# Kernel tuning notes

Measured on AMD Instinct MI355X. Metric: run time of the kernel, lower is better.

## Reference

```python
import jax, jax.numpy as jnp
import numpy as np

N_HEAD = 16
SPARSITY_K = 64


def _apply_rope(x):
    # x: [B, H, T, D]
    D = x.shape[-1]
    T = x.shape[-2]
    freqs = 1.0 / (10000.0 ** (jnp.arange(0, D, 2, dtype=jnp.float32) / D))  # [D/2]
    angles = jnp.arange(T, dtype=jnp.float32)[:, None] * freqs[None, :]      # [T, D/2]
    cos, sin = jnp.cos(angles), jnp.sin(angles)
    xe, xo = x[..., ::2], x[..., 1::2]
    re = xe * cos - xo * sin
    ro = xe * sin + xo * cos
    return jnp.stack([re, ro], axis=-1).reshape(x.shape)


def _sparse_mask(route_weights, T, k):
    # Per head h, per query t: keep positions j<=t whose route score is among
    # the top-k of route_weights[h, 0:t+1] (tie-break by smaller index, like topk).
    s = route_weights[:, :T]                      # [H, T]
    idx = jnp.arange(T)
    # G[h, jp, j] = 1 if position jp beats position j in the top-k ordering
    G = (s[:, :, None] > s[:, None, :]) | ((s[:, :, None] == s[:, None, :]) & (idx[:, None] < idx[None, :]))
    rank = jnp.cumsum(G.astype(jnp.int32), axis=1)  # rank[h, t, j] = #{jp<=t beating j}
    causal = idx[None, :, None] >= idx[None, None, :]  # j <= t
    return causal & (rank < k)                    # [H, T, T] bool


def reference(x, W_attn, b_attn, W_proj, b_proj, route_weights):
    B, T, C = x.shape
    H = N_HEAD
    D = C // H
    qkv = x @ W_attn + b_attn                     # [B, T, 3C]
    q, k, v = jnp.split(qkv, 3, axis=-1)

    def heads(t):
        return t.reshape(B, T, H, D).transpose(0, 2, 1, 3)  # [B, H, T, D]

    q, k, v = heads(q), heads(k), heads(v)
    q = _apply_rope(q)
    k = _apply_rope(k)

    scores = jnp.einsum('bhtd,bhsd->bhts', q, k) / jnp.sqrt(jnp.float32(D))
    mask = _sparse_mask(route_weights, T, SPARSITY_K)       # [H, T, T]
    scores = jnp.where(mask[None], scores, -jnp.inf)
    attn = jax.nn.softmax(scores, axis=-1)                  # dropout off (eval mode)
    out = jnp.einsum('bhts,bhsd->bhtd', attn, v)
    out = out.transpose(0, 2, 1, 3).reshape(B, T, C)
    return out @ W_proj + b_proj


def setup_inputs() -> dict:
    key = jax.random.key(0)
    ks = jax.random.split(key, 6)
    B, T, C, H = 2, 2048, 2048, 16
    return {
        'x': jax.random.normal(ks[0], (B, T, C), dtype=jnp.float32),
        'W_attn': jax.random.normal(ks[1], (C, 3 * C), dtype=jnp.float32) * 0.02,
        'b_attn': jnp.zeros((3 * C,), dtype=jnp.float32),
        'W_proj': jax.random.normal(ks[2], (C, C), dtype=jnp.float32) * 0.02,
        'b_proj': jnp.zeros((C,), dtype=jnp.float32),
        'route_weights': jax.random.normal(ks[3], (H, T), dtype=jnp.float32) * 0.02,
    }
```

## Files before the change

### kernel.cpp

```cpp
#include <hip/hip_runtime.h>
#include <stdint.h>

#define B_ 2
#define T_ 2048
#define C_ 2048
#define H_ 16
#define D_ 128
#define KSP 64
#define C3 6144

typedef __attribute__((ext_vector_type(4))) float f32x4;
typedef __attribute__((ext_vector_type(8))) _Float16 f16x8;
typedef __attribute__((ext_vector_type(4))) _Float16 f16x4;
typedef __attribute__((ext_vector_type(2))) _Float16 f16x2;

__device__ __forceinline__ void gload16(const void* g, void* l) {
  __builtin_amdgcn_global_load_lds(
      (__attribute__((address_space(1))) void*)(uintptr_t)g,
      (__attribute__((address_space(3))) void*)(uint32_t)(uintptr_t)l,
      16, 0, 0);
}

__global__ __launch_bounds__(256) void k_prep(const float* __restrict__ x,
                                              _Float16* __restrict__ x16,
                                              const float* __restrict__ Wa,
                                              _Float16* __restrict__ WaT,
                                              const float* __restrict__ Wp,
                                              _Float16* __restrict__ WpT) {
  __shared__ float tile[32][33];
  const int b = blockIdx.x;
  const int tid = threadIdx.x;
  if (b < 2048) {
    const int base = b * 4096;
#pragma unroll
    for (int p = 0; p < 4; ++p) {
      const int i = base + p * 1024 + tid * 4;
      const float4 v = *(const float4*)(x + i);
      f16x4 o;
      o.x = (_Float16)v.x; o.y = (_Float16)v.y; o.z = (_Float16)v.z; o.w = (_Float16)v.w;
      *(f16x4*)(x16 + i) = o;
    }
    return;
  }
  const float* W;
  _Float16* WT;
  int n0, k0, N;
  if (b < 14336) {
    const int t = b - 2048;
    W = Wa; WT = WaT; N = C3;
    n0 = (t % 192) * 32;
    k0 = (t / 192) * 32;
  } else {
    const int t = b - 14336;
    W = Wp; WT = WpT; N = C_;
    n0 = (t % 64) * 32;
    k0 = (t / 64) * 32;
  }
  const int tx = tid & 31, ty = tid >> 5;
#pragma unroll
  for (int r = 0; r < 4; ++r)
    tile[ty + r * 8][tx] = W[(size_t)(k0 + ty + r * 8) * N + n0 + tx];
  __syncthreads();
#pragma unroll
  for (int r = 0; r < 4; ++r)
    WT[(size_t)(n0 + ty + r * 8) * C_ + k0 + tx] = (_Float16)tile[tx][ty + r * 8];
}

template <int F16OUT, int NJ, int ROPE>
__global__ __launch_bounds__(512) void k_gemm256(const _Float16* __restrict__ A,
                                                 const _Float16* __restrict__ BT,
                                                 const float* __restrict__ bias,
                                                 void* __restrict__ Cout,
                                                 int M, int N, int K,
                                                 int RGC, int RH, int CW) {
  constexpr int BN = 64 * NJ;
  __shared__ __align__(16) _Float16 sA[2][256 * 64];
  __shared__ __align__(16) _Float16 sB[2][BN * 64];
  const int tid = threadIdx.x;
  const int lane = tid & 63;
  const int wid = tid >> 6;
  const int wr = wid >> 2;
  const int wc = wid & 3;
  const int lr = lane & 15;
  const int g = lane >> 4;
  const int rot = lr & 7;
  const int bid = blockIdx.x;
  const int x = bid & 7, q = bid >> 3;
  const int bm = (x / RGC) * RH + q / CW;
  const int bn = (x % RGC) * CW + q % CW;
  const size_t arow0 = (size_t)bm * 256;
  const size_t brow0 = (size_t)bn * BN;

  f32x4 acc[8][NJ];
#pragma unroll
  for (int mi = 0; mi < 8; ++mi)
#pragma unroll
    for (int nj = 0; nj < NJ; ++nj) acc[mi][nj] = (f32x4){0.f, 0.f, 0.f, 0.f};

  auto STAGE_A = [&](int slot, int k0) {
    const int rord[4] = {0, 2, 1, 3};
#pragma unroll
    for (int ri = 0; ri < 4; ++ri) {
      const int u = tid + rord[ri] * 512;
      const int row = u >> 3, grl = u & 7;
      const int grn = (grl - (row & 7)) & 7;
      gload16(A + (arow0 + row) * K + k0 + grn * 8, &sA[slot][u * 8]);
    }
  };
  auto STAGE_B = [&](int slot, int k0) {
#pragma unroll
    for (int r = 0; r < NJ; ++r) {
      const int u = tid + r * 512;
      const int row = u >> 3, grl = u & 7;
      const int grn = (grl - (row & 7)) & 7;
      gload16(BT + (brow0 + row) * K + k0 + grn * 8, &sB[slot][u * 8]);
    }
  };

  f16x8 af[4], bf[NJ];
  auto LDA = [&](int slot, int mh, int kk) {
#pragma unroll
    for (int mi = 0; mi < 4; ++mi) {
      const int row = wr * 128 + (mh * 4 + mi) * 16 + lr;
      af[mi] = *(const f16x8*)&sA[slot][row * 64 + (((kk * 4 + g + rot) & 7) << 3)];
    }
  };
  auto LDB = [&](int slot, int kk) {
#pragma unroll
    for (int nj = 0; nj < NJ; ++nj) {
      const int row = wc * (16 * NJ) + nj * 16 + lr;
      bf[nj] = *(const f16x8*)&sB[slot][row * 64 + (((kk * 4 + g + rot) & 7) << 3)];
    }
  };
  auto MFMAB = [&](int mh) {
    __builtin_amdgcn_s_setprio(1);
#pragma unroll
    for (int mi = 0; mi < 4; ++mi)
#pragma unroll
      for (int nj = 0; nj < NJ; ++nj)
        acc[mh * 4 + mi][nj] =
            __builtin_amdgcn_mfma_f32_16x16x32_f16(af[mi], bf[nj], acc[mh * 4 + mi][nj], 0, 0, 0);
    __builtin_amdgcn_s_setprio(0);
    __builtin_amdgcn_sched_barrier(0);
  };

  STAGE_B(0, 0);
  STAGE_A(0, 0);
  asm volatile("s_waitcnt vmcnt(2)" ::: "memory");
  __builtin_amdgcn_s_barrier();

  const int NT = K >> 6;
  for (int t = 0; t < NT; ++t) {
    const int s = t & 1, ns = s ^ 1;
    const bool pf = (t + 1 < NT);
    const int kn = (t + 1) << 6;
    LDB(s, 0);
    LDA(s, 0, 0);
    if (pf) STAGE_B(ns, kn);
    __builtin_amdgcn_s_barrier();
    asm volatile("s_waitcnt lgkmcnt(0)" ::: "memory");
    __builtin_amdgcn_sched_barrier(0);
    MFMAB(0);
    if (pf)
      asm volatile("s_waitcnt vmcnt(%0)" ::"i"(NJ) : "memory");
    else
      asm volatile("s_waitcnt vmcnt(0)" ::: "memory");
    __builtin_amdgcn_s_barrier();
    LDA(s, 1, 0);
    if (pf) STAGE_A(ns, kn);
    __builtin_amdgcn_s_barrier();
    asm volatile("s_waitcnt lgkmcnt(0)" ::: "memory");
    __builtin_amdgcn_sched_barrier(0);
    MFMAB(1);
    __builtin_amdgcn_s_barrier();
    LDB(s, 1);
    LDA(s, 0, 1);
    __builtin_amdgcn_s_barrier();
    asm volatile("s_waitcnt lgkmcnt(0)" ::: "memory");
    __builtin_amdgcn_sched_barrier(0);
    MFMAB(0);
    __builtin_amdgcn_s_barrier();
    LDA(s, 1, 1);
    __builtin_amdgcn_s_barrier();
    asm volatile("s_waitcnt lgkmcnt(0)" ::: "memory");
    __builtin_amdgcn_sched_barrier(0);
    MFMAB(1);
    if (pf)
      asm volatile("s_waitcnt vmcnt(2)" ::: "memory");
    __builtin_amdgcn_s_barrier();
  }
  const size_t row0 = arow0 + wr * 128;
  const size_t col0 = brow0 + wc * (16 * NJ);
  const float sgn = (lr & 1) ? 1.f : -1.f;
#pragma unroll
  for (int nj = 0; nj < NJ; ++nj) {
    const size_t colbase = col0 + nj * 16;
    const size_t col = colbase + lr;
    const float bv = bias[col];
    const bool dorope = ROPE && (colbase < 2 * C_);
    float freq = 0.f;
    if (dorope) {
      const int dp = ((int)(col & 127)) >> 1;
      freq = __expf(-0.14391156831212787f * (float)dp);
    }
#pragma unroll
    for (int mi = 0; mi < 8; ++mi) {
#pragma unroll
      for (int r = 0; r < 4; ++r) {
        const size_t row = row0 + mi * 16 + ((lane >> 4) << 2) + r;
        float v = acc[mi][nj][r] + bv;
        if (dorope) {
          const float pe = __shfl_xor(v, 1);
          float sn, cs;
          __sincosf((float)(int)(row & (T_ - 1)) * freq, &sn, &cs);
          v = v * cs + sgn * pe * sn;
        }
        if (F16OUT)
          ((_Float16*)Cout)[row * N + col] = (_Float16)v;
        else
          ((float*)Cout)[row * N + col] = v;
      }
    }
  }
}

__global__ __launch_bounds__(256) void k_death(const float* __restrict__ rw, int* __restrict__ dd) {
  const int widG = blockIdx.x * 4 + (threadIdx.x >> 6);
  const int lane = threadIdx.x & 63;
  const int h = widG >> 11, j = widG & (T_ - 1);
  const float* s = rw + h * T_;
  const float sj = s[j];
  int total = 0, d = T_;
  for (int base = 0; base < T_; base += 64) {
    const int t = base + lane;
    const float st = s[t];
    const bool beat = (st > sj) || (st == sj && t < j);
    const unsigned long long bal = __ballot(beat);
    const int c = __popcll(bal);
    if (total + c >= KSP) {
      const int need = KSP - total;
      const int p = __popcll(bal & ((1ull << lane) - 1ull));
      const unsigned long long win = __ballot(beat && (p == need - 1));
      d = base + __builtin_ctzll(win);
      break;
    }
    total += c;
  }
  if (lane == 0) dd[widG] = d;
}

__global__ __launch_bounds__(64) void k_slist(const int* __restrict__ dd,
                                              uint32_t* __restrict__ slist) {
  const int bid = blockIdx.x;
  const int qb = bid & 127, h = bid >> 7;
  const int i0 = qb * 16, i1 = i0 + 15;
  const int lane = threadIdx.x;
  const int* dh = dd + h * T_;
  uint32_t* lb = slist + (size_t)bid * 96;
  int total = 0;
  for (int base = 0; base <= i1; base += 64) {
    const int j = base + lane;
    const int dv = dh[j];
    const bool pred = (j <= i1) && (dv > i0);
    const unsigned long long bal = __ballot(pred);
    const int pos = total + __popcll(bal & ((1ull << lane) - 1ull));
    if (pred) lb[pos] = (uint32_t)j | ((uint32_t)dv << 12);
    total += __popcll(bal);
  }
  for (int s = total + lane; s < 96; s += 64) lb[s] = 0;
}

__global__ __launch_bounds__(64, 4) void k_mattn(const _Float16* __restrict__ qkv,
                                                 const uint32_t* __restrict__ slist,
                                                 _Float16* __restrict__ out) {
  __shared__ uint32_t jd[96];
  __shared__ int joff[96];
  __shared__ __align__(16) _Float16 Pl[16 * 104];
  __shared__ __align__(16) _Float16 VT[2048];
  const int bid = blockIdx.x;
  const int qb = bid & 127, h = (bid >> 7) & 15, b = bid >> 11;
  const int i0 = qb * 16;
  const int lane = threadIdx.x;
  const int g = lane >> 4, l = lane & 15;
  const uint32_t* lb = slist + (size_t)((h << 7) + qb) * 96;
  {
    const uint32_t pk = lb[lane];
    jd[lane] = pk;
    joff[lane] = (int)(pk & 0xFFFu) * C3;
    if (lane < 32) {
      const uint32_t pk1 = lb[64 + lane];
      jd[64 + lane] = pk1;
      joff[64 + lane] = (int)(pk1 & 0xFFFu) * C3;
    }
  }
  __syncthreads();
  const _Float16* qkvb = qkv + (size_t)b * T_ * C3;
  const _Float16* qrow = qkvb + (size_t)(i0 + l) * C3 + h * D_ + 8 * g;
  f16x8 bq[4];
#pragma unroll
  for (int c = 0; c < 4; ++c) bq[c] = *(const f16x8*)(qrow + 32 * c);
  f32x4 sacc[6];
  const _Float16* kbase = qkvb + C_ + h * D_ + 8 * g;
#pragma unroll
  for (int t = 0; t < 6; ++t) {
    const int jo = joff[16 * t + l];
    const _Float16* kr = kbase + jo;
    f16x8 ak[4];
#pragma unroll
    for (int c = 0; c < 4; ++c) ak[c] = *(const f16x8*)(kr + 32 * c);
    f32x4 a = {0.f, 0.f, 0.f, 0.f};
#pragma unroll
    for (int c = 0; c < 4; ++c)
      a = __builtin_amdgcn_mfma_f32_16x16x32_f16(ak[c], bq[c], a, 0, 0, 0);
    sacc[t] = a;
  }
  const int iq = i0 + l;
  float P[6][4];
  float m = -INFINITY;
#pragma unroll
  for (int t = 0; t < 6; ++t)
#pragma unroll
    for (int r = 0; r < 4; ++r) {
      const uint32_t pk = jd[16 * t + 4 * g + r];
      const int j = (int)(pk & 0xFFFu);
      const int d = (int)(pk >> 12);
      const bool ok = (j <= iq) && (d > iq);
      const float x = ok ? sacc[t][r] * 0.08838834764831845f : -INFINITY;
      P[t][r] = x;
      m = fmaxf(m, x);
    }
  m = fmaxf(m, __shfl_xor(m, 16));
  m = fmaxf(m, __shfl_xor(m, 32));
  float ssum = 0.f;
#pragma unroll
  for (int t = 0; t < 6; ++t)
#pragma unroll
    for (int r = 0; r < 4; ++r) {
      const float e = __expf(P[t][r] - m);
      P[t][r] = e;
      ssum += e;
    }
  ssum += __shfl_xor(ssum, 16);
  ssum += __shfl_xor(ssum, 32);
  const float inv = 1.0f / ssum;
#pragma unroll
  for (int t = 0; t < 6; ++t) {
    f16x4 w;
    w.x = (_Float16)(P[t][0] * inv);
    w.y = (_Float16)(P[t][1] * inv);
    w.z = (_Float16)(P[t][2] * inv);
    w.w = (_Float16)(P[t][3] * inv);
    *(f16x4*)&Pl[l * 104 + 16 * t + 4 * g] = w;
  }
  __syncthreads();
  f16x8 pf[3];
#pragma unroll
  for (int cc = 0; cc < 3; ++cc) pf[cc] = *(const f16x8*)&Pl[l * 104 + 32 * cc + 8 * g];
  f32x4 oacc[8];
#pragma unroll
  for (int mt = 0; mt < 8; ++mt) oacc[mt] = (f32x4){0.f, 0.f, 0.f, 0.f};
  const _Float16* vbase = qkvb + 2 * C_ + h * D_;
#pragma unroll
  for (int cc = 0; cc < 3; ++cc) {
    const int jo0 = joff[32 * cc + l];
    const int jo1 = joff[32 * cc + 16 + l];
#pragma unroll
    for (int dh = 0; dh < 2; ++dh) {
      f16x8 vl0[2], vl1[2];
#pragma unroll
      for (int cp = 0; cp < 2; ++cp) {
        vl0[cp] = *(const f16x8*)(vbase + jo0 + 64 * dh + 32 * cp + 8 * g);
        vl1[cp] = *(const f16x8*)(vbase + jo1 + 64 * dh + 32 * cp + 8 * g);
      }
      __syncthreads();
#pragma unroll
      for (int tau = 0; tau < 2; ++tau)
#pragma unroll
        for (int cp = 0; cp < 2; ++cp) {
          const int mtl = 2 * cp + (g >> 1);
          const int lt0 = 8 * (g & 1);
          const int gt = (2 * tau + (l >> 3)) ^ g;
          const int et = l & 7;
#pragma unroll
          for (int e = 0; e < 8; ++e) {
            const int idx = ((mtl * 16 + lt0 + e) * 4 + gt) * 8 + et;
            VT[idx] = tau ? vl1[cp][e] : vl0[cp][e];
          }
        }
      __syncthreads();
#pragma unroll
      for (int mtl = 0; mtl < 4; ++mtl) {
        const int sgr = (l >> 3) | ((mtl & 1) << 1);
        const f16x8 vf = *(const f16x8*)&VT[((mtl * 16 + l) * 4 + (g ^ sgr)) * 8];
        oacc[4 * dh + mtl] =
            __builtin_amdgcn_mfma_f32_16x16x32_f16(pf[cc], vf, oacc[4 * dh + mtl], 0, 0, 0);
      }
    }
  }
  _Float16* ob = out + (size_t)(b * T_ + i0 + 4 * g) * C_ + h * D_ + l;
#pragma unroll
  for (int mt = 0; mt < 8; ++mt)
#pragma unroll
    for (int r = 0; r < 4; ++r)
      ob[(size_t)r * C_ + 16 * mt] = (_Float16)oacc[mt][r];
}

extern "C" void kernel_launch(void* const* d_in, const int* in_sizes, int n_in,
                              void* d_out, int out_size, void* d_ws, size_t ws_size,
                              hipStream_t stream) {
  const float* x  = (const float*)d_in[0];
  const float* Wa = (const float*)d_in[1];
  const float* ba = (const float*)d_in[2];
  const float* Wp = (const float*)d_in[3];
  const float* bp = (const float*)d_in[4];
  const float* rw = (const float*)d_in[5];

  char* ws = (char*)d_ws;
  _Float16* qkv16 = (_Float16*)(ws);
  _Float16* WaT   = (_Float16*)(ws + (size_t)48 * 1024 * 1024);
  _Float16* WpT   = (_Float16*)(ws + (size_t)72 * 1024 * 1024);
  _Float16* x16   = (_Float16*)(ws + (size_t)80 * 1024 * 1024);
  int* dd  = (int*)(ws + (size_t)96 * 1024 * 1024);
  uint32_t* slist = (uint32_t*)(ws + (size_t)96 * 1024 * 1024 + (2 << 17));
  _Float16* att16 = x16;

  k_prep<<<dim3(18432), dim3(256), 0, stream>>>(x, x16, Wa, WaT, Wp, WpT);
  k_gemm256<1, 3, 1><<<dim3(512), dim3(512), 0, stream>>>(
      x16, WaT, ba, (void*)qkv16, B_ * T_, C3, C_, 4, 8, 8);
  k_death<<<dim3(H_ * T_ / 4), dim3(256), 0, stream>>>(rw, dd);
  k_slist<<<dim3(H_ * (T_ / 16)), dim3(64), 0, stream>>>(dd, slist);
  k_mattn<<<dim3(B_ * H_ * (T_ / 16)), dim3(64), 0, stream>>>(qkv16, slist, att16);
  k_gemm256<0, 2, 0><<<dim3(256), dim3(512), 0, stream>>>(
      att16, WpT, bp, d_out, B_ * T_, C_, C_, 4, 8, 4);
}
```

Measured before the change: 239.7 us.

## Add 128x128-tile QKV GEMM kernel with swizzled LDS and RoPE epilogue

Replaces the 256-row, 512-thread GEMM used for the QKV projection with a new 128x128 tile, 256-thread kernel. It uses a 32-wide K step, double-buffered global-to-LDS loads with an XOR-style swizzle, and 16x16x32 MFMAs, launched as 1536 blocks instead of 512. The aim is more blocks per CU and better load balance across the many CUs of the device. The cost is less data reuse per tile and a barrier on every K step. The RoPE epilogue moves into the new kernel, and the old kernel's epilogue is simplified to bias-only for the output projection, which never used RoPE.

```diff
diff --git a/kernel.cpp b/kernel.cpp
--- a/kernel.cpp
+++ b/kernel.cpp
@@ -64,6 +64,107 @@
 #pragma unroll
   for (int r = 0; r < 4; ++r)
     WT[(size_t)(n0 + ty + r * 8) * C_ + k0 + tx] = (_Float16)tile[tx][ty + r * 8];
+}
+
+template <int ROPE>
+__global__ __launch_bounds__(256, 4) void k_gemm1(const _Float16* __restrict__ A,
+                                                  const _Float16* __restrict__ BT,
+                                                  const float* __restrict__ bias,
+                                                  _Float16* __restrict__ Cout,
+                                                  int M, int N, int K,
+                                                  int RGC, int RH, int CW) {
+  __shared__ __align__(16) _Float16 sA[2][128 * 32];
+  __shared__ __align__(16) _Float16 sB[2][128 * 32];
+  const int tid = threadIdx.x;
+  const int lane = tid & 63;
+  const int wid = tid >> 6;
+  const int wr = wid >> 1;
+  const int wc = wid & 1;
+  const int lr = lane & 15;
+  const int g = lane >> 4;
+  const int bid = blockIdx.x;
+  const int x = bid & 7, q = bid >> 3;
+  const int bm = (x / RGC) * RH + q / CW;
+  const int bn = (x % RGC) * CW + q % CW;
+  const size_t arow0 = (size_t)bm * 128;
+  const size_t brow0 = (size_t)bn * 128;
+
+  f32x4 acc[4][4];
+#pragma unroll
+  for (int mi = 0; mi < 4; ++mi)
+#pragma unroll
+    for (int nj = 0; nj < 4; ++nj) acc[mi][nj] = (f32x4){0.f, 0.f, 0.f, 0.f};
+
+  auto STAGE = [&](int slot, int k0) {
+#pragma unroll
+    for (int r = 0; r < 2; ++r) {
+      const int u = tid + r * 256;
+      const int row = u >> 2, grl = u & 3;
+      const int grn = (grl - (row >> 1)) & 3;
+      gload16(A + (arow0 + row) * K + k0 + grn * 8, &sA[slot][u * 8]);
+      gload16(BT + (brow0 + row) * K + k0 + grn * 8, &sB[slot][u * 8]);
+    }
+  };
+
+  STAGE(0, 0);
+  asm volatile("s_waitcnt vmcnt(0)" ::: "memory");
+  __builtin_amdgcn_s_barrier();
+
+  const int NT = K >> 5;
+  for (int t = 0; t < NT; ++t) {
+    const int s = t & 1, ns = s ^ 1;
+    if (t + 1 < NT) STAGE(ns, (t + 1) << 5);
+    f16x8 af[4], bf[4];
+#pragma unroll
+    for (int mi = 0; mi < 4; ++mi) {
+      const int row = wr * 64 + mi * 16 + lr;
+      af[mi] = *(const f16x8*)&sA[s][row * 32 + (((g + (row >> 1)) & 3) << 3)];
+    }
+#pragma unroll
+    for (int nj = 0; nj < 4; ++nj) {
+      const int row = wc * 64 + nj * 16 + lr;
+      bf[nj] = *(const f16x8*)&sB[s][row * 32 + (((g + (row >> 1)) & 3) << 3)];
+    }
+    __builtin_amdgcn_s_setprio(1);
+#pragma unroll
+    for (int mi = 0; mi < 4; ++mi)
+#pragma unroll
+      for (int nj = 0; nj < 4; ++nj)
+        acc[mi][nj] = __builtin_amdgcn_mfma_f32_16x16x32_f16(af[mi], bf[nj], acc[mi][nj], 0, 0, 0);
+    __builtin_amdgcn_s_setprio(0);
+    asm volatile("s_waitcnt vmcnt(0)" ::: "memory");
+    __builtin_amdgcn_s_barrier();
+  }
+  const size_t row0 = arow0 + wr * 64;
+  const size_t col0 = brow0 + wc * 64;
+  const float sgn = (lr & 1) ? 1.f : -1.f;
+#pragma unroll
+  for (int nj = 0; nj < 4; ++nj) {
+    const size_t colbase = col0 + nj * 16;
+    const size_t col = colbase + lr;
+    const float bv = bias[col];
+    const bool dorope = ROPE && (colbase < 2 * C_);
+    float freq = 0.f;
+    if (dorope) {
+      const int dp = ((int)(col & 127)) >> 1;
+      freq = __expf(-0.14391156831212787f * (float)dp);
+    }
+#pragma unroll
+    for (int mi = 0; mi < 4; ++mi) {
+#pragma unroll
+      for (int r = 0; r < 4; ++r) {
+        const size_t row = row0 + mi * 16 + g * 4 + r;
+        float v = acc[mi][nj][r] + bv;
+        if (dorope) {
+          const float pe = __shfl_xor(v, 1);
+          float sn, cs;
+          __sincosf((float)(int)(row & (T_ - 1)) * freq, &sn, &cs);
+          v = v * cs + sgn * pe * sn;
+        }
+        Cout[row * N + col] = (_Float16)v;
+      }
+    }
+  }
 }
 
 template <int F16OUT, int NJ, int ROPE>
@@ -191,30 +292,16 @@
   }
   const size_t row0 = arow0 + wr * 128;
   const size_t col0 = brow0 + wc * (16 * NJ);
-  const float sgn = (lr & 1) ? 1.f : -1.f;
-#pragma unroll
-  for (int nj = 0; nj < NJ; ++nj) {
-    const size_t colbase = col0 + nj * 16;
-    const size_t col = colbase + lr;
-    const float bv = bias[col];
-    const bool dorope = ROPE && (colbase < 2 * C_);
-    float freq = 0.f;
-    if (dorope) {
-      const int dp = ((int)(col & 127)) >> 1;
-      freq = __expf(-0.14391156831212787f * (float)dp);
-    }
-#pragma unroll
-    for (int mi = 0; mi < 8; ++mi) {
+#pragma unroll
+  for (int mi = 0; mi < 8; ++mi) {
+#pragma unroll
+    for (int nj = 0; nj < NJ; ++nj) {
+      const size_t col = col0 + nj * 16 + lr;
+      const float bv = bias[col];
 #pragma unroll
       for (int r = 0; r < 4; ++r) {
-        const size_t row = row0 + mi * 16 + ((lane >> 4) << 2) + r;
-        float v = acc[mi][nj][r] + bv;
-        if (dorope) {
-          const float pe = __shfl_xor(v, 1);
-          float sn, cs;
-          __sincosf((float)(int)(row & (T_ - 1)) * freq, &sn, &cs);
-          v = v * cs + sgn * pe * sn;
-        }
+        const size_t row = row0 + mi * 16 + g * 4 + r;
+        const float v = acc[mi][nj][r] + bv;
         if (F16OUT)
           ((_Float16*)Cout)[row * N + col] = (_Float16)v;
         else
@@ -425,8 +512,8 @@
   _Float16* att16 = x16;
 
   k_prep<<<dim3(18432), dim3(256), 0, stream>>>(x, x16, Wa, WaT, Wp, WpT);
-  k_gemm256<1, 3, 1><<<dim3(512), dim3(512), 0, stream>>>(
-      x16, WaT, ba, (void*)qkv16, B_ * T_, C3, C_, 4, 8, 8);
+  k_gemm1<1><<<dim3(1536), dim3(256), 0, stream>>>(
+      x16, WaT, ba, qkv16, B_ * T_, C3, C_, 4, 16, 12);
   k_death<<<dim3(H_ * T_ / 4), dim3(256), 0, stream>>>(rw, dd);
   k_slist<<<dim3(H_ * (T_ / 16)), dim3(64), 0, stream>>>(dd, slist);
   k_mattn<<<dim3(B_ * H_ * (T_ / 16)), dim3(64), 0, stream>>>(qkv16, slist, att16);
```

After: 260.6 us. 8.7% more time.
